# Kernel tuning notes

Hardware: AMD Instinct MI355X
Metric: run time of the kernel (lower is better)

Reference implementation:

```python
import jax, jax.numpy as jnp
import numpy as np

B, L, WORD, H = 16, 32, 512, 1024
HALF = H // 2
TEMP = 1.0


def setup_inputs() -> dict:
    key = jax.random.key(0)
    ks = jax.random.split(key, 12)
    sd = 0.05
    f32 = jnp.float32
    # torch LSTMCell combined bias with forget-gate bias = 1 (gate order i,f,g,o)
    b_lstm = jnp.concatenate([jnp.zeros(HALF), jnp.ones(HALF), jnp.zeros(2 * HALF)]).astype(f32)
    return {
        "sentence_embedding": jax.random.normal(ks[0], (B, L, WORD), f32),
        "length": jax.random.randint(ks[1], (B,), L // 2, L + 1),
        "W_ih_f": jax.random.normal(ks[2], (4 * HALF, WORD), f32) * sd,
        "W_hh_f": jax.random.normal(ks[3], (4 * HALF, HALF), f32) * sd,
        "b_f": b_lstm,
        "W_ih_b": jax.random.normal(ks[4], (4 * HALF, WORD), f32) * sd,
        "W_hh_b": jax.random.normal(ks[5], (4 * HALF, HALF), f32) * sd,
        "b_b": b_lstm,
        "W_rank1": jax.random.normal(ks[6], (256, WORD + 1), f32) * sd,
        "W_rank2": jax.random.normal(ks[7], (1, 256), f32) * sd,
        "W_comp": jax.random.normal(ks[8], (5 * H, 3 * H), f32) * 0.02,
        "b_comp": jnp.zeros((5 * H,), f32),
    }


def _lstm(xs, W_ih, W_hh, b):
    # xs: (L, B, D) -> hs, cs: (B, L, HALF); torch LSTMCell gate order i,f,g,o
    n = xs.shape[1]
    hdim = W_hh.shape[1]

    def step(carry, xt):
        h, c = carry
        g = xt @ W_ih.T + h @ W_hh.T + b
        i, f, gg, o = jnp.split(g, 4, axis=1)
        c = jax.nn.sigmoid(f) * c + jax.nn.sigmoid(i) * jnp.tanh(gg)
        h = jax.nn.sigmoid(o) * jnp.tanh(c)
        return (h, c), (h, c)

    init = (jnp.zeros((n, hdim), xs.dtype), jnp.zeros((n, hdim), xs.dtype))
    _, (hs, cs) = jax.lax.scan(step, init, xs)
    return hs.transpose(1, 0, 2), cs.transpose(1, 0, 2)


def _rev_padded(x, lengths):
    # reverse the first lengths[b] timesteps of each sequence, keep padding in place
    t = np.arange(x.shape[1])
    idx = np.where(t[None, :] < lengths[:, None], lengths[:, None] - 1 - t[None, :], t[None, :])
    return jnp.take_along_axis(x, jnp.asarray(idx)[:, :, None], axis=1)


def _rank_score(seg, W1, W2):
    l = seg.shape[0]
    pos = (2.0 * jnp.arange(l, dtype=seg.dtype) / l - 1.0)[:, None]
    xy = jnp.concatenate([seg, pos], axis=1)
    return jax.nn.relu(xy @ W1.T) @ W2.T  # (l, 1)


def _compose(lst, rst, xst, Wc, bc):
    # Nary tree-LSTM composition over (left, right, current) states; None -> zeros
    hx, cx = xst
    zero = jnp.zeros_like(hx)
    hl, cl = lst if lst is not None else (zero, zero)
    hr, cr = rst if rst is not None else (zero, zero)
    g = jnp.concatenate([hl, hr, hx], axis=1) @ Wc.T + bc  # (1, 5H)
    i, fl, fr, u, o = jnp.split(g, 5, axis=1)
    c = jax.nn.sigmoid(fl) * cl + jax.nn.sigmoid(fr) * cr + jax.nn.sigmoid(i) * jnp.tanh(u)
    h = jax.nn.sigmoid(o) * jnp.tanh(c)
    return h, c


def _build(emb, hs, cs, start, end, W1, W2, Wc, bc, sent, splits, record):
    if end == start:
        return None
    if end == start + 1:
        return (hs[start:start + 1], cs[start:start + 1])
    logits_t = _rank_score(emb[start:end], W1, W2).T  # (1, l)
    y_soft = jax.nn.softmax(logits_t / TEMP, axis=1)
    if record:
        k = int(jnp.argmax(y_soft[0]))
        splits[(sent, start, end)] = k
    else:
        k = splits[(sent, start, end)]
    hard = jnp.zeros_like(y_soft).at[0, k].set(1.0)
    gate = jax.lax.stop_gradient(hard - y_soft) + y_soft  # straight-through estimator
    h = gate @ hs[start:end]
    c = gate @ cs[start:end]
    pos = start + k
    left = _build(emb, hs, cs, start, pos, W1, W2, Wc, bc, sent, splits, record)
    right = _build(emb, hs, cs, pos + 1, end, W1, W2, Wc, bc, sent, splits, record)
    return _compose(left, right, (h, c), Wc, bc)


def _forward(sentence_embedding, length, W_ih_f, W_hh_f, b_f, W_ih_b, W_hh_b, b_b,
             W_rank1, W_rank2, W_comp, b_comp, splits, record):
    lengths = np.asarray(length)
    hs_f, cs_f = _lstm(sentence_embedding.transpose(1, 0, 2), W_ih_f, W_hh_f, b_f)
    x_bw = _rev_padded(sentence_embedding, lengths)
    hs_b, cs_b = _lstm(x_bw.transpose(1, 0, 2), W_ih_b, W_hh_b, b_b)
    hs_b = _rev_padded(hs_b, lengths)
    cs_b = _rev_padded(cs_b, lengths)
    hs = jnp.concatenate([hs_f, hs_b], axis=2)  # (B, L, H)
    cs = jnp.concatenate([cs_f, cs_b], axis=2)
    h_out, c_out = [], []
    for i in range(sentence_embedding.shape[0]):
        st = _build(sentence_embedding[i], hs[i], cs[i], 0, int(lengths[i]),
                    W_rank1, W_rank2, W_comp, b_comp, i, splits, record)
        h_out.append(st[0])
        c_out.append(st[1])
    return jnp.concatenate(h_out, axis=0), jnp.concatenate(c_out, axis=0)


def reference(sentence_embedding, length, W_ih_f, W_hh_f, b_f, W_ih_b, W_hh_b, b_b,
              W_rank1, W_rank2, W_comp, b_comp):
    return _forward(sentence_embedding, length, W_ih_f, W_hh_f, b_f,
                    W_ih_b, W_hh_b, b_b, W_rank1, W_rank2, W_comp, b_comp, {}, True)
```

## Files before the change

kernel.cpp:

```cpp
#include <hip/hip_runtime.h>
#include <math.h>

#define NB 16
#define SL 32
#define H5 5120
#define K3 3072

typedef __attribute__((ext_vector_type(8))) short short8;
typedef __attribute__((ext_vector_type(4))) float floatx4;

__device__ __forceinline__ float sigf(float x) { return 1.0f / (1.0f + expf(-x)); }

__device__ __forceinline__ unsigned short f2bf(float x) {
  union { float f; unsigned int u; } v;
  v.f = x;
  unsigned int r = v.u + 0x7FFFu + ((v.u >> 16) & 1u);
  return (unsigned short)(r >> 16);
}

template <int SLP>
__device__ __forceinline__ void gbarNF(int* cnt, int* gen, int nb) {
  asm volatile("s_waitcnt vmcnt(0)" ::: "memory");
  __syncthreads();
  if (threadIdx.x == 0) {
    const int old = __hip_atomic_fetch_add(cnt, 1, __ATOMIC_RELAXED,
                                           __HIP_MEMORY_SCOPE_AGENT);
    const int g = old / nb + 1;
    if (old % nb == nb - 1) {
      __hip_atomic_store(gen, g, __ATOMIC_RELAXED, __HIP_MEMORY_SCOPE_AGENT);
    } else {
      while (__hip_atomic_load(gen, __ATOMIC_RELAXED,
                               __HIP_MEMORY_SCOPE_AGENT) < g)
        __builtin_amdgcn_s_sleep(SLP);
    }
  }
  __syncthreads();
}

__device__ __forceinline__ void gbarR(int* grp, int* gcnt, int* gen, int mygen) {
  asm volatile("s_waitcnt vmcnt(0)" ::: "memory");
  __syncthreads();
  if (threadIdx.x == 0) {
    const int g = blockIdx.x & 31;
    const int old = __hip_atomic_fetch_add(&grp[g * 16], 1, __ATOMIC_RELAXED,
                                           __HIP_MEMORY_SCOPE_AGENT);
    if ((old & 15) == 15) {
      const int og = __hip_atomic_fetch_add(gcnt, 1, __ATOMIC_RELAXED,
                                            __HIP_MEMORY_SCOPE_AGENT);
      if ((og & 31) == 31)
        __hip_atomic_store(gen, mygen, __ATOMIC_RELAXED,
                           __HIP_MEMORY_SCOPE_AGENT);
    }
    while (__hip_atomic_load(gen, __ATOMIC_RELAXED,
                             __HIP_MEMORY_SCOPE_AGENT) < mygen)
      __builtin_amdgcn_s_sleep(4);
  }
  __syncthreads();
}


__global__ void k_zero(float* __restrict__ p, int n) {
  int i = blockIdx.x * blockDim.x + threadIdx.x;
  if (i < n) p[i] = 0.0f;
}

__global__ void k_conv6(const float* s0, unsigned short* d0, int n0,
                        const float* s1, unsigned short* d1, int n1,
                        const float* s2, unsigned short* d2, int n2,
                        const float* s3, unsigned short* d3, int n3,
                        const float* s4, unsigned short* d4, int n4,
                        const float* s5, unsigned short* d5, int n5)
{
  const float* s; unsigned short* d; int n;
  switch (blockIdx.y) {
    case 0: s = s0; d = d0; n = n0; break;
    case 1: s = s1; d = d1; n = n1; break;
    case 2: s = s2; d = d2; n = n2; break;
    case 3: s = s3; d = d3; n = n3; break;
    case 4: s = s4; d = d4; n = n4; break;
    default: s = s5; d = d5; n = n5; break;
  }
  const int nf4 = n >> 2;
  for (int i = blockIdx.x * blockDim.x + threadIdx.x; i < nf4; i += gridDim.x * blockDim.x) {
    const float4 v = *(const float4*)&s[i * 4];
    ushort4 o;
    o.x = f2bf(v.x); o.y = f2bf(v.y); o.z = f2bf(v.z); o.w = f2bf(v.w);
    *(ushort4*)&d[i * 4] = o;
  }
}

__global__ __launch_bounds__(256)
void k_gemm(const float* __restrict__ A, int lda,
            const float* __restrict__ W, int ldw,
            float* __restrict__ out, int N, int K)
{
  __shared__ __align__(16) float sm[2 * 16 * 68];
  float* As = sm;
  float* Ws = sm + 16 * 68;
  const int tid = threadIdx.x;
  const int tx = tid & 15, ty = tid >> 4;
  const int g0 = blockIdx.x * 64, r0 = blockIdx.y * 64;
  float acc[4][4];
#pragma unroll
  for (int i = 0; i < 4; ++i)
#pragma unroll
    for (int j = 0; j < 4; ++j) acc[i][j] = 0.0f;
  const int ks = tid & 15, rr = tid >> 4;
  for (int kt = 0; kt < K; kt += 16) {
#pragma unroll
    for (int rep = 0; rep < 4; ++rep) {
      As[ks * 68 + rep * 16 + rr] = A[(size_t)(r0 + rep * 16 + rr) * lda + kt + ks];
      Ws[ks * 68 + rep * 16 + rr] = W[(size_t)(g0 + rep * 16 + rr) * ldw + kt + ks];
    }
    __syncthreads();
#pragma unroll
    for (int k = 0; k < 16; ++k) {
      const float4 a4 = *(const float4*)&As[k * 68 + ty * 4];
      const float4 w4 = *(const float4*)&Ws[k * 68 + tx * 4];
      const float av[4] = {a4.x, a4.y, a4.z, a4.w};
      const float wv[4] = {w4.x, w4.y, w4.z, w4.w};
#pragma unroll
      for (int i = 0; i < 4; ++i)
#pragma unroll
        for (int j = 0; j < 4; ++j) acc[i][j] += av[i] * wv[j];
    }
    __syncthreads();
  }
#pragma unroll
  for (int i = 0; i < 4; ++i) {
    const int r = r0 + ty * 4 + i;
    float4 o;
    o.x = acc[i][0]; o.y = acc[i][1]; o.z = acc[i][2]; o.w = acc[i][3];
    *(float4*)&out[(size_t)r * N + g0 + tx * 4] = o;
  }
}

__global__ __launch_bounds__(256)
void k_xproj(const unsigned short* __restrict__ embB,
             const unsigned short* __restrict__ WfB, const unsigned short* __restrict__ WbB,
             float* __restrict__ Xf, float* __restrict__ Xb)
{
  const unsigned short* B = blockIdx.z ? WbB : WfB;
  float* out = blockIdx.z ? Xb : Xf;
  __shared__ __align__(16) unsigned short As[128 * 40];
  __shared__ __align__(16) unsigned short Bs[128 * 40];
  const int tid = threadIdx.x;
  const int g0 = blockIdx.x * 128;
  const int r0 = blockIdx.y * 128;
  const int wave = tid >> 6, lane = tid & 63;
  const int wm = wave >> 1, wn = wave & 1;
  const int l15 = lane & 15, quad = lane >> 4;
  floatx4 acc[4][4];
#pragma unroll
  for (int mt = 0; mt < 4; ++mt)
#pragma unroll
    for (int nt = 0; nt < 4; ++nt) acc[mt][nt] = (floatx4){0.f, 0.f, 0.f, 0.f};
  for (int kt = 0; kt < 512; kt += 32) {
    __syncthreads();
#pragma unroll
    for (int p = 0; p < 2; ++p) {
      const int i = tid + p * 256;
      const int row = i >> 2, q = i & 3;
      *(uint4*)&As[row * 40 + q * 8] = *(const uint4*)&embB[(size_t)(r0 + row) * 512 + kt + q * 8];
      *(uint4*)&Bs[row * 40 + q * 8] = *(const uint4*)&B[(size_t)(g0 + row) * 512 + kt + q * 8];
    }
    __syncthreads();
    short8 af[4], bfr[4];
#pragma unroll
    for (int mt = 0; mt < 4; ++mt)
      af[mt] = *(const short8*)&As[(wm * 64 + mt * 16 + l15) * 40 + quad * 8];
#pragma unroll
    for (int nt = 0; nt < 4; ++nt)
      bfr[nt] = *(const short8*)&Bs[(wn * 64 + nt * 16 + l15) * 40 + quad * 8];
#pragma unroll
    for (int mt = 0; mt < 4; ++mt)
#pragma unroll
      for (int nt = 0; nt < 4; ++nt)
        acc[mt][nt] = __builtin_amdgcn_mfma_f32_16x16x32_bf16(af[mt], bfr[nt], acc[mt][nt], 0, 0, 0);
  }
#pragma unroll
  for (int nt = 0; nt < 4; ++nt) {
    const int col = g0 + wn * 64 + nt * 16 + l15;
#pragma unroll
    for (int mt = 0; mt < 4; ++mt)
#pragma unroll
      for (int i = 0; i < 4; ++i) {
        const int row = r0 + wm * 64 + mt * 16 + quad * 4 + i;
        out[(size_t)row * 2048 + col] = acc[mt][nt][i];
      }
  }
}

__global__ __launch_bounds__(256)
void k_mfma_gemm(const unsigned short* __restrict__ U, const unsigned short* __restrict__ WcB,
                 const float* __restrict__ bc, float* __restrict__ gB)
{
  __shared__ __align__(16) unsigned short As[128 * 40];
  __shared__ __align__(16) unsigned short Bs[64 * 40];
  const int bid = blockIdx.x;
  const int r0 = (bid / 80) * 128;
  const int g0 = (bid % 80) * 64;
  const int tid = threadIdx.x;
  const int wave = tid >> 6, lane = tid & 63;
  const int wm = wave >> 1, wn = wave & 1;
  const int l15 = lane & 15, quad = lane >> 4;
  floatx4 acc[4][2];
#pragma unroll
  for (int mf = 0; mf < 4; ++mf)
#pragma unroll
    for (int nt = 0; nt < 2; ++nt) acc[mf][nt] = (floatx4){0.f, 0.f, 0.f, 0.f};
  const int a_row = tid >> 2, a_q = tid & 3;
  for (int kt = 0; kt < K3; kt += 32) {
    __syncthreads();
#pragma unroll
    for (int p = 0; p < 2; ++p) {
      const int i = tid + p * 256;
      const int row = i >> 2, q = i & 3;
      *(uint4*)&As[row * 40 + q * 8] = *(const uint4*)&U[(size_t)(r0 + row) * K3 + kt + q * 8];
    }
    *(uint4*)&Bs[a_row * 40 + a_q * 8] = *(const uint4*)&WcB[(size_t)(g0 + a_row) * K3 + kt + a_q * 8];
    __syncthreads();
    short8 af[4], bfr[2];
#pragma unroll
    for (int mf = 0; mf < 4; ++mf)
      af[mf] = *(const short8*)&As[(wm * 64 + mf * 16 + l15) * 40 + quad * 8];
#pragma unroll
    for (int nt = 0; nt < 2; ++nt)
      bfr[nt] = *(const short8*)&Bs[(wn * 32 + nt * 16 + l15) * 40 + quad * 8];
#pragma unroll
    for (int mf = 0; mf < 4; ++mf)
#pragma unroll
      for (int nt = 0; nt < 2; ++nt)
        acc[mf][nt] = __builtin_amdgcn_mfma_f32_16x16x32_bf16(af[mf], bfr[nt], acc[mf][nt], 0, 0, 0);
  }
#pragma unroll
  for (int nt = 0; nt < 2; ++nt) {
    const int col = g0 + wn * 32 + nt * 16 + l15;
    const float bias = bc[col];
#pragma unroll
    for (int mf = 0; mf < 4; ++mf)
#pragma unroll
      for (int i = 0; i < 4; ++i) {
        const int row = r0 + wm * 64 + mf * 16 + quad * 4 + i;
        gB[(size_t)row * H5 + col] = acc[mf][nt][i] + bias;
      }
  }
}

__global__ __launch_bounds__(256)
void k_scan(const float* __restrict__ Xf, const float* __restrict__ Xb,
            const unsigned short* __restrict__ WhfB, const unsigned short* __restrict__ WhbB,
            const float* __restrict__ bf, const float* __restrict__ bb,
            const int* __restrict__ len,
            unsigned short* __restrict__ hbB, float* __restrict__ cbuf,
            float* __restrict__ hs, float* __restrict__ cs, int* __restrict__ bar)
{
  const int bid = blockIdx.x;
  const int dir = bid >> 5;
  const int hjt = bid & 31;
  const int tid = threadIdx.x;
  const int wave = tid >> 6, lane = tid & 63;
  const int l15 = lane & 15, quad = lane >> 4;
  const unsigned short* Wh = dir ? WhbB : WhfB;
  const float* bias = dir ? bb : bf;
  const float* X = dir ? Xb : Xf;
  int* mycnt = &bar[544 + dir * 32];
  int* mygen = &bar[560 + dir * 32];
  __shared__ float sg[4 * 16 * 17];
  const int jg = wave * 512 + hjt * 16 + l15;
  short8 wfr[16];
#pragma unroll
  for (int k8 = 0; k8 < 16; ++k8)
    wfr[k8] = *(const short8*)&Wh[(size_t)jg * 512 + k8 * 32 + quad * 8];
  const int bb_ = tid >> 4, j = tid & 15;
  const int hj = hjt * 16 + j;
  const int Lb = len[bb_];
  const float bi_i = bias[hj];
  const float bi_f = bias[512 + hj];
  const float bi_g = bias[1024 + hj];
  const float bi_o = bias[1536 + hj];
  for (int t = 0; t < SL; ++t) {
    const int pp = t & 1;
    const unsigned short* hp = hbB + (size_t)(dir * 2 + pp) * 8192;
    unsigned short* hn = hbB + (size_t)(dir * 2 + (pp ^ 1)) * 8192;
    const float* cp = cbuf + (size_t)(dir * 2 + pp) * 8192;
    float* cn = cbuf + (size_t)(dir * 2 + (pp ^ 1)) * 8192;
    short8 afr[16];
#pragma unroll
    for (int k8 = 0; k8 < 16; ++k8)
      asm volatile("global_load_dwordx4 %0, %1, off sc0 sc1"
                   : "=v"(afr[k8])
                   : "v"(&hp[(size_t)l15 * 512 + k8 * 32 + quad * 8]));
    asm volatile("s_waitcnt vmcnt(0)" ::: "memory");
    __builtin_amdgcn_sched_barrier(0);
    floatx4 acc = (floatx4){0.f, 0.f, 0.f, 0.f};
#pragma unroll
    for (int k8 = 0; k8 < 16; ++k8)
      acc = __builtin_amdgcn_mfma_f32_16x16x32_bf16(afr[k8], wfr[k8], acc, 0, 0, 0);
#pragma unroll
    for (int i = 0; i < 4; ++i)
      sg[wave * 272 + (quad * 4 + i) * 17 + l15] = acc[i];
    __syncthreads();
    int xidx = t;
    if (dir) xidx = (t < Lb) ? (Lb - 1 - t) : t;
    const float* xr = X + (size_t)(bb_ * SL + xidx) * 2048;
    const float gi = sg[0 * 272 + bb_ * 17 + j] + xr[hj] + bi_i;
    const float gf = sg[1 * 272 + bb_ * 17 + j] + xr[512 + hj] + bi_f;
    const float gg = sg[2 * 272 + bb_ * 17 + j] + xr[1024 + hj] + bi_g;
    const float go = sg[3 * 272 + bb_ * 17 + j] + xr[1536 + hj] + bi_o;
    const float cprev = cp[bb_ * 512 + hj];
    const float cnew = sigf(gf) * cprev + sigf(gi) * tanhf(gg);
    const float hnew = sigf(go) * tanhf(cnew);
    cn[bb_ * 512 + hj] = cnew;
    const unsigned int hb16 = f2bf(hnew);
    asm volatile("global_store_short %0, %1, off sc0 sc1"
                 :: "v"(&hn[bb_ * 512 + hj]), "v"(hb16) : "memory");
    const int pos = dir ? xidx : t;
    const int col = dir ? (512 + hj) : hj;
    hs[(size_t)(bb_ * SL + pos) * 1024 + col] = hnew;
    cs[(size_t)(bb_ * SL + pos) * 1024 + col] = cnew;
    if (t != SL - 1) gbarNF<4>(mycnt, mygen, 32);
  }
}

__global__ __launch_bounds__(256)
void k_score(const float* __restrict__ E1, const float* __restrict__ Wr1,
             const float* __restrict__ Wr2, const int* __restrict__ len,
             int* __restrict__ ksplit)
{
  const int b = blockIdx.x;
  const int s = blockIdx.y;
  const int L = len[b];
  if (s + 2 > L) return;
  const int tid = threadIdx.x;
  __shared__ float e[32 * 257];
  __shared__ float w1p[256];
  __shared__ float w2s[256];
  __shared__ float red[32 * 8];
  __shared__ float sc[32];
  const int nrow = 32 - s;
  for (int i = tid; i < nrow * 256; i += 256) {
    const int rr = i >> 8, q = i & 255;
    e[rr * 257 + q] = E1[(size_t)(b * SL + s + rr) * 256 + q];
  }
  w1p[tid] = Wr1[tid * 513 + 512];
  w2s[tid] = Wr2[tid];
  __syncthreads();
  const int t_ = tid & 31, jg = tid >> 5;
  const int lmax = L - s;
  for (int l = 2; l <= lmax; ++l) {
    float part = 0.0f;
    if (t_ < l) {
      const float pos = 2.0f * (float)t_ / (float)l - 1.0f;
      const float* er = e + t_ * 257;
      for (int q = jg * 32; q < jg * 32 + 32; ++q) {
        const float v = er[q] + pos * w1p[q];
        part += fmaxf(v, 0.0f) * w2s[q];
      }
    }
    red[t_ * 8 + jg] = part;
    __syncthreads();
    if (jg == 0 && t_ < l) {
      float su = 0.0f;
      for (int q = 0; q < 8; ++q) su += red[t_ * 8 + q];
      sc[t_] = su;
    }
    __syncthreads();
    if (tid == 0) {
      int k = 0;
      float best = sc[0];
      for (int q = 1; q < l; ++q)
        if (sc[q] > best) { best = sc[q]; k = q; }
      ksplit[(b * 32 + s) * 33 + l] = k;
    }
    __syncthreads();
  }
}

__global__ __launch_bounds__(64)
void k_walk(const int* __restrict__ ksplit, const int* __restrict__ len,
            int* __restrict__ meta)
{
  const int b = blockIdx.x;
  const int tid = threadIdx.x;
  __shared__ int ks[32 * 33];
  __shared__ int stk[96];
  for (int i = tid; i < 32 * 33; i += 64) ks[i] = ksplit[b * 1056 + i];
  __syncthreads();
  if (tid != 0) return;
  int* own = meta;
  int* lt = meta + 512;
  int* li = meta + 1024;
  int* rt = meta + 1536;
  int* ri = meta + 2048;
  int* dep = meta + 2560;
  int* nn = meta + 3072;
  int* dcnt = meta + 3088;
  int* lcnt = meta + 3120;
  int* dlist = meta + 3152;
  int* llist = meta + 19536;
  int sp = 0, nn_ = 1;
  stk[0] = 0; stk[1] = len[b]; stk[2] = 0;
  sp = 1;
  while (sp > 0) {
    sp--;
    const int s = stk[sp * 3], eN = stk[sp * 3 + 1], nid = stk[sp * 3 + 2];
    const int l = eN - s;
    const int k = ks[s * 33 + l];
    const int m = b * 32 + nid;
    own[m] = s + k;
    if (k == 0) { lt[m] = 0; li[m] = 0; }
    else if (k == 1) { lt[m] = 1; li[m] = s; }
    else {
      const int id = nn_++;
      lt[m] = 2; li[m] = id;
      stk[sp * 3] = s; stk[sp * 3 + 1] = s + k; stk[sp * 3 + 2] = id; sp++;
    }
    const int rl = l - k - 1;
    if (rl == 0) { rt[m] = 0; ri[m] = 0; }
    else if (rl == 1) { rt[m] = 1; ri[m] = s + k + 1; }
    else {
      const int id = nn_++;
      rt[m] = 2; ri[m] = id;
      stk[sp * 3] = s + k + 1; stk[sp * 3 + 1] = eN; stk[sp * 3 + 2] = id; sp++;
    }
  }
  nn[b] = nn_;
  for (int i = nn_ - 1; i >= 0; --i) {
    const int m = b * 32 + i;
    int d = 1;
    if (lt[m] == 2) d = max(d, dep[b * 32 + li[m]] + 1);
    if (rt[m] == 2) d = max(d, dep[b * 32 + ri[m]] + 1);
    dep[m] = d;
  }
  for (int i = 0; i < nn_; ++i) {
    const int m = b * 32 + i;
    const int r = dep[m];
    const int idx = atomicAdd(&dcnt[r], 1);
    dlist[r * 512 + idx] = m;
    if (lt[m] == 2 || rt[m] == 2) {
      const int lx = atomicAdd(&lcnt[r], 1);
      llist[r * 512 + lx] = m;
    }
  }
}

__global__ __launch_bounds__(256)
void k_ubuild(const float* __restrict__ hs, const int* __restrict__ meta,
              unsigned short* __restrict__ U)
{
  const int id = blockIdx.x, b = blockIdx.y;
  const int tid = threadIdx.x;
  const int* own = meta;
  const int* lt = meta + 512;
  const int* li = meta + 1024;
  const int* rt = meta + 1536;
  const int* ri = meta + 2048;
  const int* nn = meta + 3072;
  const int m = b * 32 + id;
  unsigned short* u = U + (size_t)m * K3;
  if (id >= nn[b]) {
    for (int i = tid; i < K3; i += 256) u[i] = 0;
    return;
  }
  const float* hl = (lt[m] == 1) ? hs + (size_t)(b * 32 + li[m]) * 1024 : nullptr;
  const float* hr = (rt[m] == 1) ? hs + (size_t)(b * 32 + ri[m]) * 1024 : nullptr;
  const float* hx = hs + (size_t)(b * 32 + own[m]) * 1024;
  for (int i = tid; i < 1024; i += 256) {
    u[i] = hl ? f2bf(hl[i]) : 0;
    u[1024 + i] = hr ? f2bf(hr[i]) : 0;
    u[2048 + i] = f2bf(hx[i]);
  }
}

__global__ __launch_bounds__(256, 2)
void k_rounds(const unsigned short* __restrict__ WcB, const int* __restrict__ meta,
              unsigned short* __restrict__ nodehb,
              const float* __restrict__ gB, const float* __restrict__ cs,
              float* __restrict__ nodec,
              float* __restrict__ out, int* __restrict__ bar,
              const unsigned short* __restrict__ zpad)
{
  const int* lt = meta + 512;
  const int* li = meta + 1024;
  const int* rt = meta + 1536;
  const int* ri = meta + 2048;
  const int* dcnt = meta + 3088;
  const int* dlist = meta + 3152;
  __shared__ float scratch[4][16][16];
  __shared__ float gates[16][16];
  const int tid = threadIdx.x;
  const int bid = blockIdx.x;
  const int wave = tid >> 6, lane = tid & 63;
  const int l15 = lane & 15, quad = lane >> 4;
  const int j0 = bid * 2;
  const int cc = (l15 < 10) ? l15 : l15 - 10;
  const size_t wrow = (size_t)((cc >> 1) * 1024 + j0 + (cc & 1)) * K3;
  const int kbase = wave * 256 + quad * 8;
  short8 wreg[16];
#pragma unroll
  for (int i = 0; i < 8; ++i) {
    wreg[i]     = *(const short8*)&WcB[wrow + kbase + i * 32];
    wreg[8 + i] = *(const short8*)&WcB[wrow + 1024 + kbase + i * 32];
  }
  const int rnd = tid >> 4, rc = tid & 15;
  int bgen = 0;
  for (int r = 1; r <= 31; ++r) {
    const int cnt = dcnt[r];
    if (cnt == 0) break;
    if (r >= 2) { ++bgen; gbarR(bar, &bar[512], &bar[528], bgen); }
    for (int c0 = 0; c0 < cnt; c0 += 16) {
      float gBv = 0.0f;
      if (rc < 10 && c0 + rnd < cnt) {
        const int nodeP = dlist[r * 512 + c0 + rnd];
        gBv = gB[(size_t)nodeP * H5 + (rc >> 1) * 1024 + j0 + (rc & 1)];
      }
      const int ma = c0 + l15;
      const unsigned short* pl = zpad;
      const unsigned short* pr = zpad;
      if (ma < cnt) {
        const int node = dlist[r * 512 + ma];
        const int base = node & ~31;
        if (lt[node] == 2) pl = nodehb + (size_t)(base + li[node]) * 1024;
        if (rt[node] == 2) pr = nodehb + (size_t)(base + ri[node]) * 1024;
      }
      short8 al[8], ar[8];
#pragma unroll
      for (int i = 0; i < 8; ++i)
        asm volatile("global_load_dwordx4 %0, %1, off sc0 sc1"
                     : "=v"(al[i]) : "v"(pl + kbase + i * 32));
#pragma unroll
      for (int i = 0; i < 8; ++i)
        asm volatile("global_load_dwordx4 %0, %1, off sc0 sc1"
                     : "=v"(ar[i]) : "v"(pr + kbase + i * 32));
      floatx4 acc = (floatx4){0.f, 0.f, 0.f, 0.f};
      asm volatile("s_waitcnt vmcnt(8)" ::: "memory");
      __builtin_amdgcn_sched_barrier(0);
#pragma unroll
      for (int ks = 0; ks < 8; ++ks)
        acc = __builtin_amdgcn_mfma_f32_16x16x32_bf16(al[ks], wreg[ks], acc, 0, 0, 0);
      asm volatile("s_waitcnt vmcnt(0)" ::: "memory");
      __builtin_amdgcn_sched_barrier(0);
#pragma unroll
      for (int ks = 0; ks < 8; ++ks)
        acc = __builtin_amdgcn_mfma_f32_16x16x32_bf16(ar[ks], wreg[8 + ks], acc, 0, 0, 0);
      __syncthreads();
#pragma unroll
      for (int i = 0; i < 4; ++i)
        scratch[wave][quad * 4 + i][l15] = acc[i];
      __syncthreads();
      if (rc < 10)
        gates[rnd][rc] = gBv + scratch[0][rnd][rc] + scratch[1][rnd][rc]
                             + scratch[2][rnd][rc] + scratch[3][rnd][rc];
      __syncthreads();
      if (tid < 16) {
        const int mc = c0 + tid;
        if (mc < cnt) {
          const int node = dlist[r * 512 + mc];
          const int base = node & ~31;
          const int ltv = lt[node], rtv = rt[node];
          const float* clp = (ltv == 2) ? &nodec[(size_t)(base + li[node]) * 1024]
                           : (ltv == 1) ? &cs[(size_t)(base + li[node]) * 1024] : nullptr;
          const float* crp = (rtv == 2) ? &nodec[(size_t)(base + ri[node]) * 1024]
                           : (rtv == 1) ? &cs[(size_t)(base + ri[node]) * 1024] : nullptr;
          unsigned int pk = 0;
#pragma unroll
          for (int jj = 0; jj < 2; ++jj) {
            const int j = j0 + jj;
            const float gi  = gates[tid][0 + jj];
            const float gfl = gates[tid][2 + jj];
            const float gfr = gates[tid][4 + jj];
            const float gu  = gates[tid][6 + jj];
            const float go  = gates[tid][8 + jj];
            const float cl = clp ? clp[j] : 0.0f;
            const float cr = crp ? crp[j] : 0.0f;
            const float c_ = sigf(gfl) * cl + sigf(gfr) * cr + sigf(gi) * tanhf(gu);
            const float h  = sigf(go) * tanhf(c_);
            nodec[(size_t)node * 1024 + j] = c_;
            pk |= ((unsigned int)f2bf(h)) << (16 * jj);
            if ((node & 31) == 0) {
              const int b = node >> 5;
              out[b * 1024 + j] = h;
              out[16384 + b * 1024 + j] = c_;
            }
          }
          asm volatile("global_store_dword %0, %1, off sc0 sc1"
                       :: "v"(nodehb + (size_t)node * 1024 + j0), "v"(pk)
                       : "memory");
        }
      }
    }
  }
}

extern "C" void kernel_launch(void* const* d_in, const int* in_sizes, int n_in,
                              void* d_out, int out_size, void* d_ws, size_t ws_size,
                              hipStream_t stream) {
  const float* emb = (const float*)d_in[0];
  const int* len = (const int*)d_in[1];
  const float* Wihf = (const float*)d_in[2];
  const float* Whhf = (const float*)d_in[3];
  const float* bf = (const float*)d_in[4];
  const float* Wihb = (const float*)d_in[5];
  const float* Whhb = (const float*)d_in[6];
  const float* bb = (const float*)d_in[7];
  const float* Wr1 = (const float*)d_in[8];
  const float* Wr2 = (const float*)d_in[9];
  const float* Wc = (const float*)d_in[10];
  const float* bc = (const float*)d_in[11];
  float* out = (float*)d_out;

  float* ws = (float*)d_ws;
  float* Xf = ws;
  float* Xb = Xf + 1048576;
  float* hs = Xb + 1048576;
  float* cs = hs + 524288;
  float* E1 = cs + 524288;
  unsigned short* U = (unsigned short*)(E1 + 131072);
  float* gB = (float*)U + 786432;
  float* nodeh = gB + 2621440;
  float* nodec = nodeh + 524288;
  unsigned short* nodehb = (unsigned short*)(nodec + 524288);
  float* cbuf = (float*)nodehb + 262144;
  unsigned short* hbB = (unsigned short*)(cbuf + 32768);
  unsigned short* WcB = (unsigned short*)((float*)hbB + 16384);
  unsigned short* WihfB = WcB + 15728640;
  unsigned short* WihbB = WihfB + 1048576;
  unsigned short* WhhfB = WihbB + 1048576;
  unsigned short* WhhbB = WhhfB + 1048576;
  unsigned short* embB = WhhbB + 1048576;
  int* meta = (int*)(embB + 262144);
  int* ksplit = meta + 36096;
  int* bar = ksplit + 16896;
  unsigned short* zpad = (unsigned short*)(bar + 1024);

  k_zero<<<192, 256, 0, stream>>>(cbuf, 49152);
  k_zero<<<1, 64, 0, stream>>>((float*)(meta + 3088), 64);
  k_zero<<<6, 256, 0, stream>>>((float*)bar, 1536);
  k_conv6<<<dim3(1920, 6), 256, 0, stream>>>(
      Wc, WcB, 15728640, Wihf, WihfB, 1048576, Wihb, WihbB, 1048576,
      Whhf, WhhfB, 1048576, Whhb, WhhbB, 1048576, emb, embB, 262144);
  k_gemm<<<dim3(4, 8), 256, 0, stream>>>(emb, 512, Wr1, 513, E1, 256, 512);
  k_xproj<<<dim3(16, 4, 2), 256, 0, stream>>>(embB, WihfB, WihbB, Xf, Xb);
  k_scan<<<64, 256, 0, stream>>>(Xf, Xb, WhhfB, WhhbB, bf, bb, len, hbB,
                                 cbuf, hs, cs, bar);
  k_score<<<dim3(16, 31), 256, 0, stream>>>(E1, Wr1, Wr2, len, ksplit);
  k_walk<<<16, 64, 0, stream>>>(ksplit, len, meta);
  k_ubuild<<<dim3(32, 16), 256, 0, stream>>>(hs, meta, U);
  k_mfma_gemm<<<320, 256, 0, stream>>>(U, WcB, bc, gB);
  k_rounds<<<512, 256, 0, stream>>>(WcB, meta, nodehb, gB, cs,
                                    nodec, out, bar, zpad);
}
```

Measured before the change: 618.6 us.

## Replace atomic-counter grid barriers with flag arrays polled by a master block

Both grid-wide barriers (the LSTM scan barrier and the tree-round barrier) stop using atomic fetch-add counters. Each block now stores its generation into its own flag slot, block 0 polls all flags with vector loads across a wavefront and then publishes the generation, and the other blocks spin on it with a shorter sleep. The scan kernel also issues the input-projection and previous-cell loads before the recurrent MFMA so their latency overlaps it. The intent is to cut barrier latency across the 32 scan steps and the tree rounds. The cost is an extra hop through the master block and a changed barrier memory layout. The early-clobber constraints on the inline asm loads are correctness fixes.

Result: faster. 606.1 us (-2.0%).

```diff
diff --git a/kernel.cpp b/kernel.cpp
--- a/kernel.cpp
+++ b/kernel.cpp
@@ -8,6 +8,7 @@
 
 typedef __attribute__((ext_vector_type(8))) short short8;
 typedef __attribute__((ext_vector_type(4))) float floatx4;
+typedef __attribute__((ext_vector_type(4))) int intx4;
 
 __device__ __forceinline__ float sigf(float x) { return 1.0f / (1.0f + expf(-x)); }
 
@@ -18,42 +19,66 @@
   return (unsigned short)(r >> 16);
 }
 
-template <int SLP>
-__device__ __forceinline__ void gbarNF(int* cnt, int* gen, int nb) {
+
+__device__ __forceinline__ void bar_scan(int* flags, int* gen, int hjt, int mygen) {
   asm volatile("s_waitcnt vmcnt(0)" ::: "memory");
   __syncthreads();
-  if (threadIdx.x == 0) {
-    const int old = __hip_atomic_fetch_add(cnt, 1, __ATOMIC_RELAXED,
-                                           __HIP_MEMORY_SCOPE_AGENT);
-    const int g = old / nb + 1;
-    if (old % nb == nb - 1) {
-      __hip_atomic_store(gen, g, __ATOMIC_RELAXED, __HIP_MEMORY_SCOPE_AGENT);
-    } else {
+  const int tid = threadIdx.x;
+  if (tid < 64) {
+    if (tid == 0)
+      __hip_atomic_store(&flags[hjt], mygen, __ATOMIC_RELAXED,
+                         __HIP_MEMORY_SCOPE_AGENT);
+    if (hjt == 0) {
+      const int off = (tid < 8) ? tid * 4 : 0;
+      int ok;
+      do {
+        intx4 f;
+        asm volatile("global_load_dwordx4 %0, %1, off sc0 sc1\n\t"
+                     "s_waitcnt vmcnt(0)"
+                     : "=&v"(f) : "v"(flags + off) : "memory");
+        ok = (f.x >= mygen) & (f.y >= mygen) & (f.z >= mygen) & (f.w >= mygen);
+      } while (__all(ok) == 0);
+      if (tid == 0)
+        __hip_atomic_store(gen, mygen, __ATOMIC_RELAXED,
+                           __HIP_MEMORY_SCOPE_AGENT);
+    } else if (tid == 0) {
       while (__hip_atomic_load(gen, __ATOMIC_RELAXED,
-                               __HIP_MEMORY_SCOPE_AGENT) < g)
-        __builtin_amdgcn_s_sleep(SLP);
+                               __HIP_MEMORY_SCOPE_AGENT) < mygen)
+        __builtin_amdgcn_s_sleep(2);
     }
   }
   __syncthreads();
 }
 
-__device__ __forceinline__ void gbarR(int* grp, int* gcnt, int* gen, int mygen) {
+__device__ __forceinline__ void bar_rounds(int* flags, int* gen, int bid, int mygen) {
   asm volatile("s_waitcnt vmcnt(0)" ::: "memory");
   __syncthreads();
-  if (threadIdx.x == 0) {
-    const int g = blockIdx.x & 31;
-    const int old = __hip_atomic_fetch_add(&grp[g * 16], 1, __ATOMIC_RELAXED,
-                                           __HIP_MEMORY_SCOPE_AGENT);
-    if ((old & 15) == 15) {
-      const int og = __hip_atomic_fetch_add(gcnt, 1, __ATOMIC_RELAXED,
-                                            __HIP_MEMORY_SCOPE_AGENT);
-      if ((og & 31) == 31)
+  const int tid = threadIdx.x;
+  if (tid < 64) {
+    if (tid == 0)
+      __hip_atomic_store(&flags[bid], mygen, __ATOMIC_RELAXED,
+                         __HIP_MEMORY_SCOPE_AGENT);
+    if (bid == 0) {
+      int ok;
+      do {
+        intx4 f0, f1;
+        asm volatile("global_load_dwordx4 %0, %2, off sc0 sc1\n\t"
+                     "global_load_dwordx4 %1, %3, off sc0 sc1\n\t"
+                     "s_waitcnt vmcnt(0)"
+                     : "=&v"(f0), "=&v"(f1)
+                     : "v"(flags + tid * 8), "v"(flags + tid * 8 + 4)
+                     : "memory");
+        ok = (f0.x >= mygen) & (f0.y >= mygen) & (f0.z >= mygen) & (f0.w >= mygen)
+           & (f1.x >= mygen) & (f1.y >= mygen) & (f1.z >= mygen) & (f1.w >= mygen);
+      } while (__all(ok) == 0);
+      if (tid == 0)
         __hip_atomic_store(gen, mygen, __ATOMIC_RELAXED,
                            __HIP_MEMORY_SCOPE_AGENT);
-    }
-    while (__hip_atomic_load(gen, __ATOMIC_RELAXED,
-                             __HIP_MEMORY_SCOPE_AGENT) < mygen)
-      __builtin_amdgcn_s_sleep(4);
+    } else if (tid == 0) {
+      while (__hip_atomic_load(gen, __ATOMIC_RELAXED,
+                               __HIP_MEMORY_SCOPE_AGENT) < mygen)
+        __builtin_amdgcn_s_sleep(2);
+    }
   }
   __syncthreads();
 }
@@ -264,8 +289,8 @@
   const unsigned short* Wh = dir ? WhbB : WhfB;
   const float* bias = dir ? bb : bf;
   const float* X = dir ? Xb : Xf;
-  int* mycnt = &bar[544 + dir * 32];
-  int* mygen = &bar[560 + dir * 32];
+  int* myflags = &bar[528 + dir * 48];
+  int* mygen = &bar[560 + dir * 48];
   __shared__ float sg[4 * 16 * 17];
   const int jg = wave * 512 + hjt * 16 + l15;
   short8 wfr[16];
@@ -285,11 +310,19 @@
     unsigned short* hn = hbB + (size_t)(dir * 2 + (pp ^ 1)) * 8192;
     const float* cp = cbuf + (size_t)(dir * 2 + pp) * 8192;
     float* cn = cbuf + (size_t)(dir * 2 + (pp ^ 1)) * 8192;
+    int xidx = t;
+    if (dir) xidx = (t < Lb) ? (Lb - 1 - t) : t;
+    const float* xr = X + (size_t)(bb_ * SL + xidx) * 2048;
+    const float x0 = xr[hj];
+    const float x1 = xr[512 + hj];
+    const float x2 = xr[1024 + hj];
+    const float x3 = xr[1536 + hj];
+    const float cprev = cp[bb_ * 512 + hj];
     short8 afr[16];
 #pragma unroll
     for (int k8 = 0; k8 < 16; ++k8)
       asm volatile("global_load_dwordx4 %0, %1, off sc0 sc1"
-                   : "=v"(afr[k8])
+                   : "=&v"(afr[k8])
                    : "v"(&hp[(size_t)l15 * 512 + k8 * 32 + quad * 8]));
     asm volatile("s_waitcnt vmcnt(0)" ::: "memory");
     __builtin_amdgcn_sched_barrier(0);
@@ -301,14 +334,10 @@
     for (int i = 0; i < 4; ++i)
       sg[wave * 272 + (quad * 4 + i) * 17 + l15] = acc[i];
     __syncthreads();
-    int xidx = t;
-    if (dir) xidx = (t < Lb) ? (Lb - 1 - t) : t;
-    const float* xr = X + (size_t)(bb_ * SL + xidx) * 2048;
-    const float gi = sg[0 * 272 + bb_ * 17 + j] + xr[hj] + bi_i;
-    const float gf = sg[1 * 272 + bb_ * 17 + j] + xr[512 + hj] + bi_f;
-    const float gg = sg[2 * 272 + bb_ * 17 + j] + xr[1024 + hj] + bi_g;
-    const float go = sg[3 * 272 + bb_ * 17 + j] + xr[1536 + hj] + bi_o;
-    const float cprev = cp[bb_ * 512 + hj];
+    const float gi = sg[0 * 272 + bb_ * 17 + j] + x0 + bi_i;
+    const float gf = sg[1 * 272 + bb_ * 17 + j] + x1 + bi_f;
+    const float gg = sg[2 * 272 + bb_ * 17 + j] + x2 + bi_g;
+    const float go = sg[3 * 272 + bb_ * 17 + j] + x3 + bi_o;
     const float cnew = sigf(gf) * cprev + sigf(gi) * tanhf(gg);
     const float hnew = sigf(go) * tanhf(cnew);
     cn[bb_ * 512 + hj] = cnew;
@@ -319,7 +348,7 @@
     const int col = dir ? (512 + hj) : hj;
     hs[(size_t)(bb_ * SL + pos) * 1024 + col] = hnew;
     cs[(size_t)(bb_ * SL + pos) * 1024 + col] = cnew;
-    if (t != SL - 1) gbarNF<4>(mycnt, mygen, 32);
+    if (t != SL - 1) bar_scan(myflags, mygen, hjt, t + 1);
   }
 }
 
@@ -508,7 +537,7 @@
   for (int r = 1; r <= 31; ++r) {
     const int cnt = dcnt[r];
     if (cnt == 0) break;
-    if (r >= 2) { ++bgen; gbarR(bar, &bar[512], &bar[528], bgen); }
+    if (r >= 2) { ++bgen; bar_rounds(bar, &bar[512], bid, bgen); }
     for (int c0 = 0; c0 < cnt; c0 += 16) {
       float gBv = 0.0f;
       if (rc < 10 && c0 + rnd < cnt) {
@@ -528,11 +557,11 @@
 #pragma unroll
       for (int i = 0; i < 8; ++i)
         asm volatile("global_load_dwordx4 %0, %1, off sc0 sc1"
-                     : "=v"(al[i]) : "v"(pl + kbase + i * 32));
+                     : "=&v"(al[i]) : "v"(pl + kbase + i * 32));
 #pragma unroll
       for (int i = 0; i < 8; ++i)
         asm volatile("global_load_dwordx4 %0, %1, off sc0 sc1"
-                     : "=v"(ar[i]) : "v"(pr + kbase + i * 32));
+                     : "=&v"(ar[i]) : "v"(pr + kbase + i * 32));
       floatx4 acc = (floatx4){0.f, 0.f, 0.f, 0.f};
       asm volatile("s_waitcnt vmcnt(8)" ::: "memory");
       __builtin_amdgcn_sched_barrier(0);
```
